# Kernel tuning notes

Measured on AMD Instinct MI355X. Metric: run time of the kernel, lower is better.

## Reference

```python
import jax, jax.numpy as jnp
import numpy as np

N_HEADS = 6
HEAD_SIZE = 64


def setup_inputs() -> dict:
    key = jax.random.key(0)
    k1, k2, k3, k4 = jax.random.split(key, 4)
    B, T, C = 8, 2048, N_HEADS * HEAD_SIZE
    x = jax.random.normal(k1, (B, T, C), dtype=jnp.float32)
    # small init scale keeps softmax logits in a sane range
    w_qkv = jax.random.normal(k2, (C, 3 * C), dtype=jnp.float32) * 0.05
    w_proj = jax.random.normal(k3, (C, C), dtype=jnp.float32) * 0.05
    b_proj = jax.random.normal(k4, (C,), dtype=jnp.float32) * 0.05
    return {"x": x, "w_qkv": w_qkv, "w_proj": w_proj, "b_proj": b_proj}


def reference(x, w_qkv, w_proj, b_proj):
    B, T, C = x.shape
    qkv = x @ w_qkv                      # [B, T, 3C]
    q, k, v = jnp.split(qkv, 3, axis=2)
    # [B, T, C] -> [B, H, T, D]
    def heads(t):
        return t.reshape(B, T, N_HEADS, HEAD_SIZE).transpose(0, 2, 1, 3)
    q, k, v = heads(q), heads(k), heads(v)
    scale = HEAD_SIZE ** -0.5
    scores = jnp.einsum('bhqd,bhkd->bhqk', q, k) * scale   # [B, H, T, T]
    causal = jnp.tril(jnp.ones((T, T), dtype=bool))
    scores = jnp.where(causal[None, None], scores, jnp.float32(-jnp.inf))
    weights = jax.nn.softmax(scores, axis=-1)
    # dropout is identity in eval mode
    out = jnp.einsum('bhqk,bhkd->bhqd', weights, v)          # [B, H, T, D]
    out = out.transpose(0, 2, 1, 3).reshape(B, T, C)
    return out @ w_proj + b_proj
```

## Files before the change

### kernel.cpp

```cpp
#include <hip/hip_runtime.h>
#include <hip/hip_bf16.h>

typedef __bf16 bf16_t;
typedef __bf16 bf16x8 __attribute__((ext_vector_type(8)));
typedef __bf16 bf16x4 __attribute__((ext_vector_type(4)));
typedef float floatx4 __attribute__((ext_vector_type(4)));

#define MFMA16(a, b, c) __builtin_amdgcn_mfma_f32_16x16x32_bf16(a, b, c, 0, 0, 0)

#if __has_builtin(__builtin_amdgcn_exp2f)
#define EXP2F(x) __builtin_amdgcn_exp2f(x)
#else
#define EXP2F(x) __expf((x)*0.693147180559945f)
#endif

__device__ __forceinline__ void async_copy16(const bf16_t* g, bf16_t* l) {
    __builtin_amdgcn_global_load_lds((const __attribute__((address_space(1))) void*)g,
                                     (__attribute__((address_space(3))) void*)l, 16, 0, 0);
}

__global__ void prep_fused(const float* __restrict__ x, const float* __restrict__ w_qkv,
                           const float* __restrict__ w_proj, bf16_t* __restrict__ xb,
                           bf16_t* __restrict__ wqkvT, bf16_t* __restrict__ wprojT) {
    const int bx = blockIdx.x, tid = threadIdx.x;
    if (bx < 3072) {
        size_t i = ((size_t)bx * 256 + tid) * 8;
        float4 v0 = *(const float4*)(x + i);
        float4 v1 = *(const float4*)(x + i + 4);
        bf16x8 o = {(bf16_t)v0.x, (bf16_t)v0.y, (bf16_t)v0.z, (bf16_t)v0.w,
                    (bf16_t)v1.x, (bf16_t)v1.y, (bf16_t)v1.z, (bf16_t)v1.w};
        *(bf16x8*)(xb + i) = o;
        return;
    }
    __shared__ float tile[32][33];
    int which, n0, k0, Nd;
    if (bx < 3072 + 432) {
        int idx = bx - 3072;
        which = 0; Nd = 1152; n0 = (idx % 36) * 32; k0 = (idx / 36) * 32;
    } else {
        int idx = bx - 3072 - 432;
        which = 1; Nd = 384; n0 = (idx % 12) * 32; k0 = (idx / 12) * 32;
    }
    const float* in = which ? w_proj : w_qkv;
    bf16_t* out = which ? wprojT : wqkvT;
    const int tx = tid & 31, ty = tid >> 5;
#pragma unroll
    for (int i = 0; i < 4; i++)
        tile[ty + i * 8][tx] = in[(size_t)(k0 + ty + i * 8) * Nd + n0 + tx];
    __syncthreads();
#pragma unroll
    for (int i = 0; i < 4; i++) {
        int n = n0 + ty + i * 8;
        float v = tile[tx][ty + i * 8];
        if (!which && n < 384) v *= 0.1803368851f;
        out[(size_t)n * 384 + k0 + tx] = (bf16_t)v;
    }
}

__global__ __launch_bounds__(256, 3)
void gemm_qkv(const bf16_t* __restrict__ A, const bf16_t* __restrict__ Bt,
              bf16_t* __restrict__ qkv, bf16_t* __restrict__ Vt, int M, int N, int K) {
    __shared__ __align__(16) bf16_t As[2][128 * 32];
    __shared__ __align__(16) bf16_t Bs[2][128 * 32];
    const int tid = threadIdx.x;
    const int wave = tid >> 6, lane = tid & 63;
    const int wm = wave >> 1, wn = wave & 1;
    const int quad = lane >> 4, l16 = lane & 15;
    const int row0 = blockIdx.y * 128, col0 = blockIdx.x * 128;
    const int swz = l16 & 3;

    floatx4 acc[4][4];
#pragma unroll
    for (int i = 0; i < 4; i++)
#pragma unroll
        for (int j = 0; j < 4; j++) acc[i][j] = (floatx4){0.f, 0.f, 0.f, 0.f};

    auto stage = [&](int buf, int k0) {
#pragma unroll
        for (int it = 0; it < 2; it++) {
            int cb = wave * 64 + it * 256;
            int c = cb + lane;
            int r = c >> 2;
            int col = k0 + (((c & 3) ^ (r & 3)) * 8);
            async_copy16(A + (size_t)(row0 + r) * K + col, &As[buf][0] + cb * 8);
            async_copy16(Bt + (size_t)(col0 + r) * K + col, &Bs[buf][0] + cb * 8);
        }
    };

    const int nk = K >> 5;
    stage(0, 0);
    for (int kt = 0; kt < nk; kt++) {
        __syncthreads();
        if (kt + 1 < nk) stage((kt + 1) & 1, (kt + 1) * 32);
        const bf16_t* as = &As[kt & 1][0];
        const bf16_t* bs = &Bs[kt & 1][0];
        bf16x8 af[4], bfr[4];
#pragma unroll
        for (int i = 0; i < 4; i++)
            af[i] = *(const bf16x8*)(as + (wm * 64 + i * 16 + l16) * 32 + ((quad ^ swz) * 8));
#pragma unroll
        for (int j = 0; j < 4; j++)
            bfr[j] = *(const bf16x8*)(bs + (wn * 64 + j * 16 + l16) * 32 + ((quad ^ swz) * 8));
#pragma unroll
        for (int i = 0; i < 4; i++)
#pragma unroll
            for (int j = 0; j < 4; j++) acc[i][j] = MFMA16(bfr[j], af[i], acc[i][j]);
    }
    if (col0 < 768) {
#pragma unroll
        for (int i = 0; i < 4; i++) {
            const size_t row = (size_t)(row0 + wm * 64 + i * 16 + l16);
#pragma unroll
            for (int j = 0; j < 4; j++) {
                const int colb = col0 + wn * 64 + j * 16 + quad * 4;
                bf16x4 v = {(bf16_t)acc[i][j][0], (bf16_t)acc[i][j][1],
                            (bf16_t)acc[i][j][2], (bf16_t)acc[i][j][3]};
                *(bf16x4*)(qkv + row * N + colb) = v;
            }
        }
    } else {
#pragma unroll
        for (int i = 0; i < 4; i++) {
            const int row = row0 + wm * 64 + i * 16 + l16;
            const int b = row >> 11, t = row & 2047;
#pragma unroll
            for (int j = 0; j < 4; j++) {
                const int vcol = col0 - 768 + wn * 64 + j * 16 + quad * 4;
                const int h = vcol >> 6, d = vcol & 63;
                bf16_t* vp = Vt + (((size_t)(b * 6 + h) * 64 + d) << 11) + t;
#pragma unroll
                for (int r = 0; r < 4; r++) vp[(size_t)r << 11] = (bf16_t)acc[i][j][r];
            }
        }
    }
}

__global__ __launch_bounds__(256, 3)
void gemm_out(const bf16_t* __restrict__ A, const bf16_t* __restrict__ Bt,
              float* __restrict__ C, int M, int N, int K, const float* __restrict__ bias) {
    __shared__ __align__(16) bf16_t As[2][128 * 32];
    __shared__ __align__(16) bf16_t Bs[2][64 * 32];
    const int tid = threadIdx.x;
    const int wave = tid >> 6, lane = tid & 63;
    const int wm = wave >> 1, wn = wave & 1;
    const int quad = lane >> 4, l16 = lane & 15;
    const int row0 = blockIdx.y * 128, col0 = blockIdx.x * 64;
    const int swz = l16 & 3;

    floatx4 acc[4][2];
#pragma unroll
    for (int i = 0; i < 4; i++)
#pragma unroll
        for (int j = 0; j < 2; j++) acc[i][j] = (floatx4){0.f, 0.f, 0.f, 0.f};

    auto stage = [&](int buf, int k0) {
#pragma unroll
        for (int it = 0; it < 2; it++) {
            int cb = wave * 64 + it * 256;
            int c = cb + lane;
            int r = c >> 2;
            int col = k0 + (((c & 3) ^ (r & 3)) * 8);
            async_copy16(A + (size_t)(row0 + r) * K + col, &As[buf][0] + cb * 8);
            if (it == 0)
                async_copy16(Bt + (size_t)(col0 + r) * K + col, &Bs[buf][0] + cb * 8);
        }
    };

    const int nk = K >> 5;
    stage(0, 0);
    for (int kt = 0; kt < nk; kt++) {
        __syncthreads();
        if (kt + 1 < nk) stage((kt + 1) & 1, (kt + 1) * 32);
        const bf16_t* as = &As[kt & 1][0];
        const bf16_t* bs = &Bs[kt & 1][0];
        bf16x8 af[4], bfr[2];
#pragma unroll
        for (int i = 0; i < 4; i++)
            af[i] = *(const bf16x8*)(as + (wm * 64 + i * 16 + l16) * 32 + ((quad ^ swz) * 8));
#pragma unroll
        for (int j = 0; j < 2; j++)
            bfr[j] = *(const bf16x8*)(bs + (wn * 32 + j * 16 + l16) * 32 + ((quad ^ swz) * 8));
#pragma unroll
        for (int i = 0; i < 4; i++)
#pragma unroll
            for (int j = 0; j < 2; j++) acc[i][j] = MFMA16(bfr[j], af[i], acc[i][j]);
    }
#pragma unroll
    for (int i = 0; i < 4; i++) {
        const size_t row = (size_t)(row0 + wm * 64 + i * 16 + l16);
#pragma unroll
        for (int j = 0; j < 2; j++) {
            const int colb = col0 + wn * 32 + j * 16 + quad * 4;
            float4 bv = *(const float4*)(bias + colb);
            float4 v = {acc[i][j][0] + bv.x, acc[i][j][1] + bv.y,
                        acc[i][j][2] + bv.z, acc[i][j][3] + bv.w};
            *(float4*)(C + row * N + colb) = v;
        }
    }
}

__device__ __forceinline__ void stage64(const bf16_t* __restrict__ gtile, int stride,
                                        bf16_t* lds, int wave, int lane) {
#pragma unroll
    for (int it = 0; it < 2; it++) {
        int cb = wave * 64 + it * 256;
        int c = cb + lane;
        int r = c >> 3;
        int col = ((c & 7) ^ (r & 7)) * 8;
        async_copy16(gtile + (size_t)r * stride + col, lds + cb * 8);
    }
}

__global__ __launch_bounds__(256, 3)
void attn_kernel(const bf16_t* __restrict__ qkv, const bf16_t* __restrict__ Vt,
                 bf16_t* __restrict__ attn_out) {
    constexpr int T = 2048, C3 = 1152;
    const int bx = blockIdx.x, h = blockIdx.y, b = blockIdx.z;
    const int qa = bx, qb = 31 - bx;
    const int tid = threadIdx.x;
    const int wave = tid >> 6, lane = tid & 63;
    const int quad = lane >> 4, l16 = lane & 15;

    __shared__ __align__(16) bf16_t Ks[2][64 * 64];
    __shared__ __align__(16) bf16_t Vs[2][64 * 64];
    __shared__ __align__(16) bf16_t Ps[4][2][16 * 64];

    const bf16_t* kbase = qkv + (size_t)b * T * C3 + 384 + h * 64;
    const bf16_t* vbase = Vt + ((size_t)(b * 6 + h)) * 64 * T;

    const bf16_t* qpa =
        qkv + ((size_t)b * T + qa * 64 + wave * 16 + l16) * C3 + h * 64 + quad * 8;
    const bf16_t* qpb =
        qkv + ((size_t)b * T + qb * 64 + wave * 16 + l16) * C3 + h * 64 + quad * 8;
    bf16x8 qA0 = *(const bf16x8*)qpa, qA1 = *(const bf16x8*)(qpa + 32);
    bf16x8 qB0 = *(const bf16x8*)qpb, qB1 = *(const bf16x8*)(qpb + 32);

    floatx4 oA[4], oB[4];
    float lpA = 0.f, lpB = 0.f;
#pragma unroll
    for (int r = 0; r < 4; r++) {
        oA[r] = (floatx4){0.f, 0.f, 0.f, 0.f};
        oB[r] = (floatx4){0.f, 0.f, 0.f, 0.f};
    }
    const floatx4 C0 = {-13.f, -13.f, -13.f, -13.f};

    stage64(kbase, C3, &Ks[0][0], wave, lane);
    stage64(vbase, T, &Vs[0][0], wave, lane);

    const int swz = l16 & 7;
    bf16_t* psA = &Ps[wave][0][0];
    bf16_t* psB = &Ps[wave][1][0];

    for (int kt = 0; kt <= qb; kt++) {
        __syncthreads();
        if (kt < qb) {
            stage64(kbase + (size_t)(kt + 1) * 64 * C3, C3, &Ks[(kt + 1) & 1][0], wave, lane);
            stage64(vbase + (kt + 1) * 64, T, &Vs[(kt + 1) & 1][0], wave, lane);
        }
        const bf16_t* kb = &Ks[kt & 1][0];
        const bf16_t* vb = &Vs[kt & 1][0];
        const bool doA = (kt <= qa);

        bf16x8 kf[4][2];
#pragma unroll
        for (int nt = 0; nt < 4; nt++)
#pragma unroll
            for (int hh = 0; hh < 2; hh++)
                kf[nt][hh] = *(const bf16x8*)(kb + (nt * 16 + l16) * 64 +
                                              (((hh * 4 + quad) ^ swz) * 8));

        floatx4 sA[4], sB[4];
#pragma unroll
        for (int nt = 0; nt < 4; nt++) {
            sB[nt] = MFMA16(kf[nt][0], qB0, C0);
            sB[nt] = MFMA16(kf[nt][1], qB1, sB[nt]);
        }
        if (doA) {
#pragma unroll
            for (int nt = 0; nt < 4; nt++) {
                sA[nt] = MFMA16(kf[nt][0], qA0, C0);
                sA[nt] = MFMA16(kf[nt][1], qA1, sA[nt]);
            }
        }
        if (kt == qb) {
#pragma unroll
            for (int nt = 0; nt < 4; nt++)
#pragma unroll
                for (int r = 0; r < 4; r++)
                    if (nt * 16 + quad * 4 + r > wave * 16 + l16) sB[nt][r] = -1e30f;
        }
        if (kt == qa) {
#pragma unroll
            for (int nt = 0; nt < 4; nt++)
#pragma unroll
                for (int r = 0; r < 4; r++)
                    if (nt * 16 + quad * 4 + r > wave * 16 + l16) sA[nt][r] = -1e30f;
        }

#pragma unroll
        for (int nt = 0; nt < 4; nt++) {
#pragma unroll
            for (int r = 0; r < 4; r++) {
                float p = EXP2F(sB[nt][r]);
                sB[nt][r] = p;
                lpB += p;
            }
            bf16x4 p4 = {(bf16_t)sB[nt][0], (bf16_t)sB[nt][1],
                         (bf16_t)sB[nt][2], (bf16_t)sB[nt][3]};
            *(bf16x4*)(psB + l16 * 64 + (((nt * 2 + (quad >> 1)) ^ swz) * 8) +
                       (quad & 1) * 4) = p4;
        }
        if (doA) {
#pragma unroll
            for (int nt = 0; nt < 4; nt++) {
#pragma unroll
                for (int r = 0; r < 4; r++) {
                    float p = EXP2F(sA[nt][r]);
                    sA[nt][r] = p;
                    lpA += p;
                }
                bf16x4 p4 = {(bf16_t)sA[nt][0], (bf16_t)sA[nt][1],
                             (bf16_t)sA[nt][2], (bf16_t)sA[nt][3]};
                *(bf16x4*)(psA + l16 * 64 + (((nt * 2 + (quad >> 1)) ^ swz) * 8) +
                           (quad & 1) * 4) = p4;
            }
        }

        bf16x8 vf[4][2];
#pragma unroll
        for (int nt = 0; nt < 4; nt++)
#pragma unroll
            for (int hh = 0; hh < 2; hh++)
                vf[nt][hh] = *(const bf16x8*)(vb + (nt * 16 + l16) * 64 +
                                              (((hh * 4 + quad) ^ swz) * 8));

        asm volatile("s_waitcnt lgkmcnt(0)" ::: "memory");

        bf16x8 pB0 = *(const bf16x8*)(psB + l16 * 64 + ((quad ^ swz) * 8));
        bf16x8 pB1 = *(const bf16x8*)(psB + l16 * 64 + (((4 + quad) ^ swz) * 8));
#pragma unroll
        for (int dt = 0; dt < 4; dt++) {
            oB[dt] = MFMA16(vf[dt][0], pB0, oB[dt]);
            oB[dt] = MFMA16(vf[dt][1], pB1, oB[dt]);
        }
        if (doA) {
            bf16x8 pA0 = *(const bf16x8*)(psA + l16 * 64 + ((quad ^ swz) * 8));
            bf16x8 pA1 = *(const bf16x8*)(psA + l16 * 64 + (((4 + quad) ^ swz) * 8));
#pragma unroll
            for (int dt = 0; dt < 4; dt++) {
                oA[dt] = MFMA16(vf[dt][0], pA0, oA[dt]);
                oA[dt] = MFMA16(vf[dt][1], pA1, oA[dt]);
            }
        }
    }

    lpA += __shfl_xor(lpA, 16); lpA += __shfl_xor(lpA, 32);
    lpB += __shfl_xor(lpB, 16); lpB += __shfl_xor(lpB, 32);
    const float invA = 1.0f / lpA, invB = 1.0f / lpB;
    const int tA = qa * 64 + wave * 16 + l16, tB = qb * 64 + wave * 16 + l16;
#pragma unroll
    for (int dt = 0; dt < 4; dt++) {
        bf16x4 va = {(bf16_t)(oA[dt][0] * invA), (bf16_t)(oA[dt][1] * invA),
                     (bf16_t)(oA[dt][2] * invA), (bf16_t)(oA[dt][3] * invA)};
        bf16x4 vb4 = {(bf16_t)(oB[dt][0] * invB), (bf16_t)(oB[dt][1] * invB),
                      (bf16_t)(oB[dt][2] * invB), (bf16_t)(oB[dt][3] * invB)};
        int col = h * 64 + dt * 16 + quad * 4;
        *(bf16x4*)(attn_out + ((size_t)b * T + tA) * 384 + col) = va;
        *(bf16x4*)(attn_out + ((size_t)b * T + tB) * 384 + col) = vb4;
    }
}

extern "C" void kernel_launch(void* const* d_in, const int* in_sizes, int n_in,
                              void* d_out, int out_size, void* d_ws, size_t ws_size,
                              hipStream_t stream) {
    const float* x      = (const float*)d_in[0];
    const float* w_qkv  = (const float*)d_in[1];
    const float* w_proj = (const float*)d_in[2];
    const float* b_proj = (const float*)d_in[3];
    float* out = (float*)d_out;

    bf16_t* ws = (bf16_t*)d_ws;
    bf16_t* wqkvT = ws;
    bf16_t* wprojT = wqkvT + 1152 * 384;
    bf16_t* xb = wprojT + 384 * 384;
    bf16_t* qkv = xb + (size_t)16384 * 384;
    bf16_t* Vt = qkv + (size_t)16384 * 1152;
    bf16_t* attn = Vt + (size_t)48 * 64 * 2048;

    hipLaunchKernelGGL(prep_fused, dim3(3072 + 432 + 144), dim3(256), 0, stream,
                       x, w_qkv, w_proj, xb, wqkvT, wprojT);
    hipLaunchKernelGGL(gemm_qkv, dim3(9, 128), dim3(256), 0, stream,
                       xb, wqkvT, qkv, Vt, 16384, 1152, 384);
    hipLaunchKernelGGL(attn_kernel, dim3(16, 6, 8), dim3(256), 0, stream, qkv, Vt, attn);
    hipLaunchKernelGGL(gemm_out, dim3(6, 128), dim3(256), 0, stream,
                       attn, wprojT, out, 16384, 384, 384, b_proj);
}
```

Before: 182.0 us.

## Store transposed V in contiguous 64x64 tiles via LDS-staged coalesced writes

```diff
diff --git a/kernel.cpp b/kernel.cpp
--- a/kernel.cpp
+++ b/kernel.cpp
@@ -119,18 +119,31 @@
             }
         }
     } else {
-#pragma unroll
-        for (int i = 0; i < 4; i++) {
-            const int row = row0 + wm * 64 + i * 16 + l16;
-            const int b = row >> 11, t = row & 2047;
-#pragma unroll
-            for (int j = 0; j < 4; j++) {
-                const int vcol = col0 - 768 + wn * 64 + j * 16 + quad * 4;
-                const int h = vcol >> 6, d = vcol & 63;
-                bf16_t* vp = Vt + (((size_t)(b * 6 + h) * 64 + d) << 11) + t;
-#pragma unroll
-                for (int r = 0; r < 4; r++) vp[(size_t)r << 11] = (bf16_t)acc[i][j][r];
-            }
+        __syncthreads();
+        bf16_t* myb = &As[0][0] + wave * 4096;
+#pragma unroll
+        for (int i = 0; i < 4; i++)
+#pragma unroll
+            for (int j = 0; j < 4; j++)
+#pragma unroll
+                for (int r = 0; r < 4; r++) {
+                    int d2 = j * 16 + quad * 4 + r;
+                    int t2 = i * 16 + l16;
+                    myb[d2 * 64 + (((t2 >> 3) ^ (d2 & 7)) * 8) + (t2 & 7)] =
+                        (bf16_t)acc[i][j][r];
+                }
+        asm volatile("s_waitcnt lgkmcnt(0)" ::: "memory");
+        const int row_t = row0 + wm * 64;
+        const int b = row_t >> 11;
+        const int tt = (row_t & 2047) >> 6;
+        const int h = (col0 - 768 + wn * 64) >> 6;
+        bf16_t* vout = Vt + (((size_t)(b * 6 + h) * 32 + tt) << 12);
+#pragma unroll
+        for (int it = 0; it < 8; it++) {
+            int d2 = it * 8 + (lane >> 3);
+            int cl = lane & 7;
+            bf16x8 v = *(const bf16x8*)(myb + d2 * 64 + ((cl ^ (d2 & 7)) * 8));
+            *(bf16x8*)(vout + d2 * 64 + cl * 8) = v;
         }
     }
 }
@@ -226,7 +239,7 @@
     __shared__ __align__(16) bf16_t Ps[4][2][16 * 64];
 
     const bf16_t* kbase = qkv + (size_t)b * T * C3 + 384 + h * 64;
-    const bf16_t* vbase = Vt + ((size_t)(b * 6 + h)) * 64 * T;
+    const bf16_t* vbase = Vt + (((size_t)(b * 6 + h) * 32) << 12);
 
     const bf16_t* qpa =
         qkv + ((size_t)b * T + qa * 64 + wave * 16 + l16) * C3 + h * 64 + quad * 8;
@@ -245,7 +258,7 @@
     const floatx4 C0 = {-13.f, -13.f, -13.f, -13.f};
 
     stage64(kbase, C3, &Ks[0][0], wave, lane);
-    stage64(vbase, T, &Vs[0][0], wave, lane);
+    stage64(vbase, 64, &Vs[0][0], wave, lane);
 
     const int swz = l16 & 7;
     bf16_t* psA = &Ps[wave][0][0];
@@ -255,7 +268,7 @@
         __syncthreads();
         if (kt < qb) {
             stage64(kbase + (size_t)(kt + 1) * 64 * C3, C3, &Ks[(kt + 1) & 1][0], wave, lane);
-            stage64(vbase + (kt + 1) * 64, T, &Vs[(kt + 1) & 1][0], wave, lane);
+            stage64(vbase + ((kt + 1) << 12), 64, &Vs[(kt + 1) & 1][0], wave, lane);
         }
         const bf16_t* kb = &Ks[kt & 1][0];
         const bf16_t* vb = &Vs[kt & 1][0];
```

Result: no change. 180.4 us (-0.9%).
